# Kernel optimization log

Hardware: AMD Instinct MI355X
Metric: run time of the kernel (lower is better)

## Reference

```python
import jax, jax.numpy as jnp
import numpy as np

DIM = 3          # algebra dimension (3D Clifford algebra Cl(3,0))
NB = 2 ** DIM    # 8 blades
C_IN, C_OUT = 4, 4
K = 3            # conv kernel size
S = 48           # spatial size (== mask_size)
B = 4            # batch size
HID = 128


def _build_algebra():
    """Cayley table of Cl(3,0) with blades ordered by (grade, bitmask), and the
    path matrix M[p, bj, bk] = sum_bi cayley[bi,bj,bk] restricted to grade-triple p."""
    n = NB
    blades = sorted(range(n), key=lambda b: (bin(b).count('1'), b))
    idx = {b: i for i, b in enumerate(blades)}
    grades = np.array([bin(b).count('1') for b in blades])
    cay = np.zeros((n, n, n), dtype=np.float32)
    for a in range(n):
        for b in range(n):
            s = 1
            t = a >> 1
            while t:
                s *= (-1) ** bin(t & b).count('1')
                t >>= 1
            cay[idx[a], idx[b], idx[a ^ b]] = s  # Euclidean metric: no extra signs
    ng = DIM + 1
    path_id = -np.ones((ng, ng, ng), dtype=int)
    p = 0
    for gi in range(ng):
        for gj in range(ng):
            for gk in range(ng):
                if np.any(cay[np.ix_(np.where(grades == gi)[0], np.where(grades == gj)[0], np.where(grades == gk)[0])] != 0):
                    path_id[gi, gj, gk] = p
                    p += 1
    P = p  # == product_paths_sum == 20 for Cl(3,0)
    M = np.zeros((P, n, n), dtype=np.float32)
    for i in range(n):
        for j in range(n):
            for k in range(n):
                c = cay[i, j, k]
                if c != 0.0:
                    M[path_id[grades[i], grades[j], grades[k]], j, k] += c
    return M, P

CAYLEY_M, P = _build_algebra()


def _circular_mask(ks):
    c = (ks - 1) / 2.0
    zz, yy, xx = np.ogrid[:ks, :ks, :ks]
    d = np.sqrt((xx - c) ** 2 + (yy - c) ** 2 + (zz - c) ** 2)
    return (d <= c).astype(np.float32)


def _rel_pos_mv():
    """Kernel-grid offsets embedded as grade-1 multivectors: (K^3, NB)."""
    ax = np.linspace(-1.0, 1.0, K).astype(np.float32)
    gx, gy, gz = np.meshgrid(ax, ax, ax, indexing='ij')
    pos = np.stack([gx, gy, gz], -1).reshape(-1, DIM)
    mv = np.zeros((K ** DIM, NB), dtype=np.float32)
    mv[:, 1:1 + DIM] = pos  # grade-1 blade slots are indices 1..3
    return mv


def setup_inputs() -> dict:
    key = jax.random.key(0)
    ks = jax.random.split(key, 4)
    x = jax.random.normal(ks[0], (B, C_IN, S, S, S, NB), jnp.float32)
    w0 = jax.random.normal(ks[1], (2 * NB, HID), jnp.float32) / np.sqrt(2 * NB)
    w1 = jax.random.normal(ks[2], (HID, HID), jnp.float32) / np.sqrt(HID)
    w2 = jax.random.normal(ks[3], (HID, C_OUT * C_IN * P), jnp.float32) / np.sqrt(HID)
    return {
        'x': x,
        'w0': w0, 'b0': jnp.zeros((HID,), jnp.float32),
        'w1': w1, 'b1': jnp.zeros((HID,), jnp.float32),
        'w2': w2, 'b2': jnp.zeros((C_OUT * C_IN * P,), jnp.float32),
        'bias_param': jnp.zeros((C_OUT, 1, 1, 1, 1), jnp.float32),
    }


def reference(x, w0, b0, w1, b1, w2, b2, bias_param):
    # 1) masked global pooling -> per-sample per-blade condition (B, NB)
    mask = jnp.asarray(_circular_mask(S))
    cond = jnp.einsum('bcxyzn,xyz->bn', x, mask) / (mask.sum() * C_IN)

    # 2) per-sample dynamic kernel generation (vmapped kernel network)
    rel = jnp.asarray(_rel_pos_mv())               # (X, NB), X = K^3
    X = K ** DIM
    feat = jnp.concatenate([
        jnp.broadcast_to(rel[None], (B, X, NB)),
        jnp.broadcast_to(cond[:, None, :], (B, X, NB)),
    ], axis=-1)                                     # (B, X, 2*NB)
    h = jax.nn.gelu(feat @ w0 + b0)
    h = jax.nn.gelu(h @ w1 + b1)
    w = (h @ w2 + b2).reshape(B, X, C_OUT, C_IN, P)  # per-path geometric-product weights

    # 3) assemble blade-level kernel via sparse Cayley contraction
    M = jnp.asarray(CAYLEY_M)                       # (P, NB_in_blade, NB_out_blade)
    ker = jnp.einsum('bxoip,pjk->bokijx', w, M)     # (B, o, bk, i, bj, X)
    kernels = ker.reshape(B * C_OUT * NB, C_IN * NB, K, K, K)

    # 4) grouped conv: one kernel bank per sample (feature_group_count = B)
    inp = jnp.transpose(x, (0, 1, 5, 2, 3, 4)).reshape(1, B * C_IN * NB, S, S, S)
    out = jax.lax.conv_general_dilated(
        inp, kernels, window_strides=(1, 1, 1), padding='SAME',
        dimension_numbers=('NCDHW', 'OIDHW', 'NCDHW'), feature_group_count=B)
    out = out.reshape(B, C_OUT, NB, S, S, S)
    out = jnp.transpose(out, (0, 1, 3, 4, 5, 2))    # (B, c_out, S,S,S, NB)

    # 5) multivector bias embedded at blade dims (0,)
    bias = jnp.zeros((C_OUT, 1, 1, 1, NB), x.dtype).at[..., 0:1].set(bias_param)
    return out + bias
```

## Files before the change

### kernel.cpp

```cpp
#include <hip/hip_runtime.h>
#include <cmath>

#define SS 48
#define S3 110592
#define NB 8
#define CIN 4
#define COUT 4
#define HID 128
#define XT 27
#define NP 20
#define BATCH 4
#define PD 50
#define PD2 2500
#define PD3 125000
#define SLABV 648
#define SLABS 5184

typedef __attribute__((ext_vector_type(8))) short short8;
typedef __attribute__((ext_vector_type(4))) float f32x4;

struct Tables {
    int   pid[64];
    float sgn[64];
};

__device__ __forceinline__ unsigned short bf16_rne(float f) {
    union { float f; unsigned u; } c; c.f = f;
    unsigned r = c.u + 0x7FFF + ((c.u >> 16) & 1);
    return (unsigned short)(r >> 16);
}

__device__ __forceinline__ float gelu_tanh(float v) {
    const float c = 0.7978845608028654f;
    float u = c * (v + 0.044715f * v * v * v);
    return 0.5f * v * (1.0f + tanhf(u));
}

__global__ __launch_bounds__(256)
void pack_cond_kernel(const float* __restrict__ x, unsigned short* __restrict__ xb,
                      float* __restrict__ partial) {
    int b  = blockIdx.y;
    int pv = blockIdx.x * 256 + threadIdx.x;
    __shared__ float sacc[8];
    if (threadIdx.x < 8) sacc[threadIdx.x] = 0.0f;
    __syncthreads();
    float acc[8];
#pragma unroll
    for (int n = 0; n < 8; ++n) acc[n] = 0.0f;
    if (pv < PD3) {
        int zp = pv / PD2, rem = pv % PD2, yp = rem / PD, xp = rem % PD;
        int z = zp - 1, y = yp - 1, xx = xp - 1;
        unsigned short ob[32];
        bool interior = (unsigned)z < 48u && (unsigned)y < 48u && (unsigned)xx < 48u;
        if (interior) {
            int v = (z * 48 + y) * 48 + xx;
            float vals[32];
#pragma unroll
            for (int i = 0; i < 4; ++i) {
                const f32x4* p = (const f32x4*)(x + (((size_t)(b * 4 + i)) * S3 + v) * 8);
                f32x4 a = p[0], c4 = p[1];
                vals[i * 8 + 0] = a[0];  vals[i * 8 + 1] = a[1];
                vals[i * 8 + 2] = a[2];  vals[i * 8 + 3] = a[3];
                vals[i * 8 + 4] = c4[0]; vals[i * 8 + 5] = c4[1];
                vals[i * 8 + 6] = c4[2]; vals[i * 8 + 7] = c4[3];
            }
            int dx = 2 * xx - 47, dy = 2 * y - 47, dz = 2 * z - 47;
            if (dx * dx + dy * dy + dz * dz <= 2209) {
#pragma unroll
                for (int n = 0; n < 8; ++n)
                    acc[n] = vals[n] + vals[8 + n] + vals[16 + n] + vals[24 + n];
            }
#pragma unroll
            for (int k = 0; k < 32; ++k) ob[k] = bf16_rne(vals[k]);
        } else {
#pragma unroll
            for (int k = 0; k < 32; ++k) ob[k] = 0;
        }
        short8* dst = (short8*)(xb + ((size_t)b * PD3 + pv) * 32);
#pragma unroll
        for (int q = 0; q < 4; ++q) {
            short8 s;
#pragma unroll
            for (int e = 0; e < 8; ++e) s[e] = (short)ob[q * 8 + e];
            dst[q] = s;
        }
    }
#pragma unroll
    for (int n = 0; n < 8; ++n) {
        float a = acc[n];
        for (int off = 32; off; off >>= 1) a += __shfl_down(a, off);
        if ((threadIdx.x & 63) == 0) atomicAdd(&sacc[n], a);
    }
    __syncthreads();
    if (threadIdx.x < 8)
        partial[((size_t)b * 512 + blockIdx.x) * 8 + threadIdx.x] = sacc[threadIdx.x];
}

__global__ __launch_bounds__(320)
void mlp_fused(const float* __restrict__ partial,
               const float* __restrict__ w0, const float* __restrict__ b0,
               const float* __restrict__ w1, const float* __restrict__ b1,
               const float* __restrict__ w2, const float* __restrict__ b2,
               unsigned short* __restrict__ wb, float inv_norm, Tables tb) {
    int bx = blockIdx.x;
    int b = bx / XT, tap = bx % XT;
    int t = threadIdx.x;
    __shared__ float red[40][8];
    __shared__ float feat[16];
    __shared__ float h1[HID];
    __shared__ float h2[HID];
    __shared__ float wrow[320];
    {
        int ch = t & 7, seg = t >> 3;
        float s = 0.0f;
        for (int j = seg; j < 489; j += 40)
            s += partial[((size_t)b * 512 + j) * 8 + ch];
        red[seg][ch] = s;
    }
    __syncthreads();
    if (t < 8) {
        float s2 = 0.0f;
#pragma unroll
        for (int q = 0; q < 40; ++q) s2 += red[q][t];
        feat[8 + t] = s2 * inv_norm;
        float v = 0.0f;
        if (t == 1) v = (float)(tap / 9) - 1.0f;
        else if (t == 2) v = (float)((tap / 3) % 3) - 1.0f;
        else if (t == 3) v = (float)(tap % 3) - 1.0f;
        feat[t] = v;
    }
    __syncthreads();
    if (t < 128) {
        float s = b0[t];
#pragma unroll
        for (int k = 0; k < 16; ++k) s += feat[k] * w0[k * HID + t];
        h1[t] = gelu_tanh(s);
    }
    __syncthreads();
    if (t < 128) {
        float a0 = b1[t], a1 = 0.0f, a2 = 0.0f, a3 = 0.0f;
#pragma unroll
        for (int k = 0; k < HID; k += 4) {
            a0 += h1[k + 0] * w1[(k + 0) * HID + t];
            a1 += h1[k + 1] * w1[(k + 1) * HID + t];
            a2 += h1[k + 2] * w1[(k + 2) * HID + t];
            a3 += h1[k + 3] * w1[(k + 3) * HID + t];
        }
        h2[t] = gelu_tanh((a0 + a1) + (a2 + a3));
    }
    __syncthreads();
    {
        float a0 = b2[t], a1 = 0.0f, a2 = 0.0f, a3 = 0.0f;
#pragma unroll
        for (int k = 0; k < HID; k += 4) {
            a0 += h2[k + 0] * w2[(size_t)(k + 0) * 320 + t];
            a1 += h2[k + 1] * w2[(size_t)(k + 1) * 320 + t];
            a2 += h2[k + 2] * w2[(size_t)(k + 2) * 320 + t];
            a3 += h2[k + 3] * w2[(size_t)(k + 3) * 320 + t];
        }
        wrow[t] = (a0 + a1) + (a2 + a3);
    }
    __syncthreads();
    if (t < 128) {
        int m = t >> 2, cq = t & 3;
        int o = m >> 3, bk = m & 7;
        short8 sv;
#pragma unroll
        for (int e = 0; e < 8; ++e) {
            int c = cq * 8 + e;
            int i = c >> 3, bj = c & 7, jk = bj * 8 + bk;
            sv[e] = (short)bf16_rne(tb.sgn[jk] * wrow[o * 80 + i * 20 + tb.pid[jk]]);
        }
        int g  = (tap / 9) * 3 + (tap % 3);
        int ky = (tap % 9) / 3;
        int half = m >> 4, mm = m & 15;
        size_t tile = (size_t)(b * 27 + g * 3 + ky) * 1024;
        *(short8*)(wb + tile + half * 512 + (mm + cq * 16) * 8) = sv;
    }
}

__global__ __launch_bounds__(512, 2)
void conv_lds(const unsigned short* __restrict__ xb, const unsigned short* __restrict__ wb,
              const float* __restrict__ bias, float* __restrict__ out) {
    __shared__ __align__(16) short lds[2][4 * SLABS];
    int bid = blockIdx.x;
    int tid = threadIdx.x, lane = tid & 63, wave = tid >> 6;
    int zs = wave >> 1, mh = wave & 1;
    int col = lane & 15, kl = lane >> 4;

    int b = bid >> 6, k = bid & 63;
    int start, cntt;
    if (k < 48) { start = k * 7; cntt = 7; }
    else        { start = 336 + (k - 48) * 6; cntt = 6; }

    const unsigned short* xbb = xb + (size_t)b * PD3 * 32;

    const unsigned short* wgl = wb + (size_t)b * 27648 + mh * 512 + lane * 8;
    short8 wreg[27];
#pragma unroll
    for (int t27 = 0; t27 < 27; ++t27) {
        const unsigned short* p = wgl + (size_t)t27 * 1024;
        asm volatile("global_load_dwordx4 %0, %1, off" : "=v"(wreg[t27]) : "v"(p));
    }

    int sl = wave >> 1, hbase = (wave & 1) * 324;
    auto stage = [&](int tau, int buf) {
        int txx = tau % 3, tyy = (tau / 3) % 12, tzz = tau / 36;
        const unsigned short* base = xbb +
            ((size_t)(tzz * 4) * PD2 + (size_t)(tyy * 4) * PD + txx * 16) * 32 + sl * 8;
#pragma unroll
        for (int kk = 0; kk < 6; ++kk) {
            int h0 = hbase + kk * 64;
            int h  = h0 + lane;
            if (h < hbase + 324) {
                int hz = h / 108, rem = h % 108, hy = rem / 18, hx = rem % 18;
                __builtin_amdgcn_global_load_lds(
                    (const unsigned int*)(base + ((size_t)hz * PD2 + hy * PD + hx) * 32),
                    (unsigned int*)&lds[buf][sl * SLABS + h0 * 8], 16, 0, 0);
            }
        }
    };

    stage(start, 0);
    __syncthreads();

    for (int i = 0; i < cntt; ++i) {
        int tau = start + i;
        if (i + 1 < cntt) stage(tau + 1, (i + 1) & 1);

        int txx = tau % 3, tyy = (tau / 3) % 12, tzz = tau / 36;
        const short* lbase = &lds[i & 1][kl * SLABS + (zs * 108 + col) * 8];

        f32x4 acc[4];
#pragma unroll
        for (int r = 0; r < 4; ++r)
#pragma unroll
            for (int e = 0; e < 4; ++e) acc[r][e] = 0.0f;

#pragma unroll
        for (int kz = 0; kz < 3; ++kz)
#pragma unroll
            for (int kx = 0; kx < 3; ++kx) {
                const short* lb = lbase + (kz * 108 + kx) * 8;
                short8 bfv[6];
#pragma unroll
                for (int u = 0; u < 6; ++u)
                    bfv[u] = *(const short8*)(lb + u * 144);
#pragma unroll
                for (int ky = 0; ky < 3; ++ky) {
                    short8 a = wreg[(kz * 3 + kx) * 3 + ky];
#pragma unroll
                    for (int r = 0; r < 4; ++r)
                        acc[r] = __builtin_amdgcn_mfma_f32_16x16x32_bf16(a, bfv[r + ky], acc[r], 0, 0, 0);
                }
            }

        int xc = txx * 16 + col;
        int z  = tzz * 4 + zs;
        int m0 = kl * 4 + mh * 16;
        int o = m0 >> 3, bk0 = m0 & 7;
        float bi = (bk0 == 0) ? bias[o] : 0.0f;
#pragma unroll
        for (int r = 0; r < 4; ++r) {
            int y = tyy * 4 + r;
            int vox = (z * 48 + y) * 48 + xc;
            f32x4 v = acc[r];
            v[0] += bi;
            *(f32x4*)(out + (((size_t)(b * 4 + o)) * S3 + vox) * 8 + bk0) = v;
        }
        __syncthreads();
    }
}

static inline int pc_host(int v) { return __builtin_popcount(v); }

extern "C" void kernel_launch(void* const* d_in, const int* in_sizes, int n_in,
                              void* d_out, int out_size, void* d_ws, size_t ws_size,
                              hipStream_t stream) {
    const float* x    = (const float*)d_in[0];
    const float* w0   = (const float*)d_in[1];
    const float* b0   = (const float*)d_in[2];
    const float* w1   = (const float*)d_in[3];
    const float* b1   = (const float*)d_in[4];
    const float* w2   = (const float*)d_in[5];
    const float* b2   = (const float*)d_in[6];
    const float* bias = (const float*)d_in[7];
    float* out = (float*)d_out;

    float* ws      = (float*)d_ws;
    float* partial = ws;
    unsigned short* wbb = (unsigned short*)(ws + 30272);
    unsigned short* xb  = wbb + 110592;

    int cnt = 0;
    for (int z = 0; z < SS; ++z) {
        int dz = 2 * z - 47;
        for (int y = 0; y < SS; ++y) {
            int dy = 2 * y - 47;
            for (int xx = 0; xx < SS; ++xx) {
                int dx = 2 * xx - 47;
                if (dx * dx + dy * dy + dz * dz <= 2209) ++cnt;
            }
        }
    }
    float inv_norm = 1.0f / ((float)cnt * (float)CIN);

    int pidtab[4][4][4];
    {
        bool ex[4][4][4] = {};
        for (int A = 0; A < 8; ++A)
            for (int B = 0; B < 8; ++B)
                ex[pc_host(A)][pc_host(B)][pc_host(A ^ B)] = true;
        int p = 0;
        for (int gi = 0; gi < 4; ++gi)
            for (int gj = 0; gj < 4; ++gj)
                for (int gk = 0; gk < 4; ++gk)
                    pidtab[gi][gj][gk] = ex[gi][gj][gk] ? p++ : -1;
    }
    static const int blades[8] = {0, 1, 2, 4, 3, 5, 6, 7};
    Tables tb;
    for (int bj = 0; bj < 8; ++bj) {
        for (int bk = 0; bk < 8; ++bk) {
            int bmj = blades[bj], bmk = blades[bk];
            int bma = bmj ^ bmk;
            int sgn = 1, t = bma >> 1;
            while (t) {
                if (pc_host(t & bmj) & 1) sgn = -sgn;
                t >>= 1;
            }
            tb.sgn[bj * 8 + bk] = (float)sgn;
            tb.pid[bj * 8 + bk] = pidtab[pc_host(bma)][pc_host(bmj)][pc_host(bmk)];
        }
    }

    pack_cond_kernel<<<dim3(489, BATCH), dim3(256), 0, stream>>>(x, xb, partial);
    mlp_fused<<<dim3(BATCH * XT), dim3(320), 0, stream>>>(partial, w0, b0, w1, b1, w2, b2,
                                                          wbb, inv_norm, tb);
    conv_lds<<<dim3(256), dim3(512), 0, stream>>>(xb, wbb, bias, out);
}
```

Before: 63.29 us.

## Split border zeroing from packing, double-buffer LDS fragment loads, relax occupancy

The pack kernel now iterates over interior voxels only and no longer branches on padding. A separate kernel zeroes the padded border, and the MLP reduction now sums 432 partials. In the conv kernel, B-operand LDS loads for the next tap group are issued into alternating register buffers while the current MFMAs run, with s_setprio raising priority around the MFMA bursts. Launch bounds drop to one block per CU to give the extra buffer registers room. The cost is an extra kernel launch and possibly lower occupancy.

```diff
diff --git a/kernel.cpp b/kernel.cpp
--- a/kernel.cpp
+++ b/kernel.cpp
@@ -37,53 +37,51 @@
 }
 
 __global__ __launch_bounds__(256)
+void border_kernel(unsigned short* __restrict__ xb) {
+    int b  = blockIdx.y;
+    int pv = blockIdx.x * 256 + threadIdx.x;
+    if (pv >= PD3) return;
+    int zp = pv / PD2, rem = pv % PD2, yp = rem / PD, xp = rem % PD;
+    if (zp == 0 || zp == 49 || yp == 0 || yp == 49 || xp == 0 || xp == 49) {
+        short8 z8 = {0, 0, 0, 0, 0, 0, 0, 0};
+        short8* dst = (short8*)(xb + ((size_t)b * PD3 + pv) * 32);
+        dst[0] = z8; dst[1] = z8; dst[2] = z8; dst[3] = z8;
+    }
+}
+
+__global__ __launch_bounds__(256)
 void pack_cond_kernel(const float* __restrict__ x, unsigned short* __restrict__ xb,
                       float* __restrict__ partial) {
-    int b  = blockIdx.y;
-    int pv = blockIdx.x * 256 + threadIdx.x;
+    int b = blockIdx.y;
+    int v = blockIdx.x * 256 + threadIdx.x;
     __shared__ float sacc[8];
     if (threadIdx.x < 8) sacc[threadIdx.x] = 0.0f;
     __syncthreads();
+    int z = v / 2304, rem = v % 2304, y = rem / 48, xx = rem % 48;
+    float vals[32];
+#pragma unroll
+    for (int i = 0; i < 4; ++i) {
+        const f32x4* p = (const f32x4*)(x + (((size_t)(b * 4 + i)) * S3 + v) * 8);
+        f32x4 a = p[0], c4 = p[1];
+        vals[i * 8 + 0] = a[0];  vals[i * 8 + 1] = a[1];
+        vals[i * 8 + 2] = a[2];  vals[i * 8 + 3] = a[3];
+        vals[i * 8 + 4] = c4[0]; vals[i * 8 + 5] = c4[1];
+        vals[i * 8 + 6] = c4[2]; vals[i * 8 + 7] = c4[3];
+    }
     float acc[8];
-#pragma unroll
-    for (int n = 0; n < 8; ++n) acc[n] = 0.0f;
-    if (pv < PD3) {
-        int zp = pv / PD2, rem = pv % PD2, yp = rem / PD, xp = rem % PD;
-        int z = zp - 1, y = yp - 1, xx = xp - 1;
-        unsigned short ob[32];
-        bool interior = (unsigned)z < 48u && (unsigned)y < 48u && (unsigned)xx < 48u;
-        if (interior) {
-            int v = (z * 48 + y) * 48 + xx;
-            float vals[32];
-#pragma unroll
-            for (int i = 0; i < 4; ++i) {
-                const f32x4* p = (const f32x4*)(x + (((size_t)(b * 4 + i)) * S3 + v) * 8);
-                f32x4 a = p[0], c4 = p[1];
-                vals[i * 8 + 0] = a[0];  vals[i * 8 + 1] = a[1];
-                vals[i * 8 + 2] = a[2];  vals[i * 8 + 3] = a[3];
-                vals[i * 8 + 4] = c4[0]; vals[i * 8 + 5] = c4[1];
-                vals[i * 8 + 6] = c4[2]; vals[i * 8 + 7] = c4[3];
-            }
-            int dx = 2 * xx - 47, dy = 2 * y - 47, dz = 2 * z - 47;
-            if (dx * dx + dy * dy + dz * dz <= 2209) {
-#pragma unroll
-                for (int n = 0; n < 8; ++n)
-                    acc[n] = vals[n] + vals[8 + n] + vals[16 + n] + vals[24 + n];
-            }
-#pragma unroll
-            for (int k = 0; k < 32; ++k) ob[k] = bf16_rne(vals[k]);
-        } else {
-#pragma unroll
-            for (int k = 0; k < 32; ++k) ob[k] = 0;
-        }
-        short8* dst = (short8*)(xb + ((size_t)b * PD3 + pv) * 32);
-#pragma unroll
-        for (int q = 0; q < 4; ++q) {
-            short8 s;
-#pragma unroll
-            for (int e = 0; e < 8; ++e) s[e] = (short)ob[q * 8 + e];
-            dst[q] = s;
-        }
+    int dx = 2 * xx - 47, dy = 2 * y - 47, dz = 2 * z - 47;
+    bool inmask = (dx * dx + dy * dy + dz * dz <= 2209);
+#pragma unroll
+    for (int n = 0; n < 8; ++n)
+        acc[n] = inmask ? (vals[n] + vals[8 + n] + vals[16 + n] + vals[24 + n]) : 0.0f;
+
+    short8* dst = (short8*)(xb + ((size_t)b * PD3 + (size_t)(z + 1) * PD2 + (y + 1) * PD + (xx + 1)) * 32);
+#pragma unroll
+    for (int q = 0; q < 4; ++q) {
+        short8 s;
+#pragma unroll
+        for (int e = 0; e < 8; ++e) s[e] = (short)bf16_rne(vals[q * 8 + e]);
+        dst[q] = s;
     }
 #pragma unroll
     for (int n = 0; n < 8; ++n) {
@@ -113,7 +111,7 @@
     {
         int ch = t & 7, seg = t >> 3;
         float s = 0.0f;
-        for (int j = seg; j < 489; j += 40)
+        for (int j = seg; j < 432; j += 40)
             s += partial[((size_t)b * 512 + j) * 8 + ch];
         red[seg][ch] = s;
     }
@@ -179,7 +177,7 @@
     }
 }
 
-__global__ __launch_bounds__(512, 2)
+__global__ __launch_bounds__(512, 1)
 void conv_lds(const unsigned short* __restrict__ xb, const unsigned short* __restrict__ wb,
               const float* __restrict__ bias, float* __restrict__ out) {
     __shared__ __align__(16) short lds[2][4 * SLABS];
@@ -237,23 +235,48 @@
 #pragma unroll
             for (int e = 0; e < 4; ++e) acc[r][e] = 0.0f;
 
-#pragma unroll
-        for (int kz = 0; kz < 3; ++kz)
-#pragma unroll
-            for (int kx = 0; kx < 3; ++kx) {
-                const short* lb = lbase + (kz * 108 + kx) * 8;
-                short8 bfv[6];
-#pragma unroll
-                for (int u = 0; u < 6; ++u)
-                    bfv[u] = *(const short8*)(lb + u * 144);
+        short8 bfA[6], bfB[6];
+#pragma unroll
+        for (int u = 0; u < 6; ++u)
+            bfA[u] = *(const short8*)(lbase + u * 144);
+
+#pragma unroll
+        for (int g = 0; g < 9; ++g) {
+            const int kzn = (g + 1) / 3, kxn = (g + 1) % 3;
+            if ((g & 1) == 0) {
+                if (g < 8) {
+                    const short* lb = lbase + (kzn * 108 + kxn) * 8;
+#pragma unroll
+                    for (int u = 0; u < 6; ++u)
+                        bfB[u] = *(const short8*)(lb + u * 144);
+                }
+                __builtin_amdgcn_s_setprio(1);
 #pragma unroll
                 for (int ky = 0; ky < 3; ++ky) {
-                    short8 a = wreg[(kz * 3 + kx) * 3 + ky];
+                    short8 a = wreg[g * 3 + ky];
 #pragma unroll
                     for (int r = 0; r < 4; ++r)
-                        acc[r] = __builtin_amdgcn_mfma_f32_16x16x32_bf16(a, bfv[r + ky], acc[r], 0, 0, 0);
+                        acc[r] = __builtin_amdgcn_mfma_f32_16x16x32_bf16(a, bfA[r + ky], acc[r], 0, 0, 0);
                 }
+                __builtin_amdgcn_s_setprio(0);
+            } else {
+                if (g < 8) {
+                    const short* lb = lbase + (kzn * 108 + kxn) * 8;
+#pragma unroll
+                    for (int u = 0; u < 6; ++u)
+                        bfA[u] = *(const short8*)(lb + u * 144);
+                }
+                __builtin_amdgcn_s_setprio(1);
+#pragma unroll
+                for (int ky = 0; ky < 3; ++ky) {
+                    short8 a = wreg[g * 3 + ky];
+#pragma unroll
+                    for (int r = 0; r < 4; ++r)
+                        acc[r] = __builtin_amdgcn_mfma_f32_16x16x32_bf16(a, bfB[r + ky], acc[r], 0, 0, 0);
+                }
+                __builtin_amdgcn_s_setprio(0);
             }
+        }
 
         int xc = txx * 16 + col;
         int z  = tzz * 4 + zs;
@@ -333,7 +356,8 @@
         }
     }
 
-    pack_cond_kernel<<<dim3(489, BATCH), dim3(256), 0, stream>>>(x, xb, partial);
+    border_kernel<<<dim3(489, BATCH), dim3(256), 0, stream>>>(xb);
+    pack_cond_kernel<<<dim3(432, BATCH), dim3(256), 0, stream>>>(x, xb, partial);
     mlp_fused<<<dim3(BATCH * XT), dim3(320), 0, stream>>>(partial, w0, b0, w1, b1, w2, b2,
                                                           wbb, inv_norm, tb);
     conv_lds<<<dim3(256), dim3(512), 0, stream>>>(xb, wbb, bias, out);
```

Measured after the change: 66.71 us. 1.05x slower.
